# Kernel tuning notes

Hardware: AMD Instinct MI355X
Metric: run time of the kernel (lower is better)

Reference implementation:

```python
import jax, jax.numpy as jnp
import numpy as np

EPS = 1e-5
OUTPUT_BINS = 1000


def _act_quant(x):
    # per-token absmax int8 quantization (BitNet b1.58)
    scale = 127.0 / jnp.clip(jnp.max(jnp.abs(x), axis=-1, keepdims=True), EPS, None)
    return jnp.clip(jnp.round(x * scale), -128.0, 127.0) / scale


def _weight_quant(w):
    # ternary absmean quantization
    scale = 1.0 / jnp.clip(jnp.mean(jnp.abs(w)), EPS, None)
    return jnp.clip(jnp.round(w * scale), -1.0, 1.0) / scale


def _ste(x, q):
    return x + jax.lax.stop_gradient(q - x)


def bitlinear(x, w):
    xq = _ste(x, _act_quant(x))
    wq = _ste(w, _weight_quant(w))
    return jnp.einsum('bi,oi->bo', xq, wq)


def layernorm(x, g, b):
    mu = jnp.mean(x, axis=-1, keepdims=True)
    var = jnp.mean(jnp.square(x - mu), axis=-1, keepdims=True)
    return (x - mu) * jax.lax.rsqrt(var + EPS) * g + b


def setup_inputs() -> dict:
    key = jax.random.key(0)
    ks = jax.random.split(key, 5)
    B, D_IN, H = 4096, 1024, 4096
    return {
        'x': jax.random.normal(ks[0], (B, D_IN), dtype=jnp.float32),
        'W0': jax.random.normal(ks[1], (H, D_IN), dtype=jnp.float32) * 0.02,
        'W1': jax.random.normal(ks[2], (H, H), dtype=jnp.float32) * 0.02,
        'W2': jax.random.normal(ks[3], (H, H), dtype=jnp.float32) * 0.02,
        'W3': jax.random.normal(ks[4], (2 * OUTPUT_BINS, H), dtype=jnp.float32) * 0.02,
        'g0': jnp.ones((H,), jnp.float32), 'b0': jnp.zeros((H,), jnp.float32),
        'g1': jnp.ones((H,), jnp.float32), 'b1': jnp.zeros((H,), jnp.float32),
        'g2': jnp.ones((H,), jnp.float32), 'b2': jnp.zeros((H,), jnp.float32),
    }


def reference(x, W0, W1, W2, W3, g0, b0, g1, b1, g2, b2):
    h = jax.nn.silu(layernorm(bitlinear(x, W0), g0, b0))
    h = jax.nn.silu(layernorm(bitlinear(h, W1), g1, b1))
    h = jax.nn.silu(layernorm(bitlinear(h, W2), g2, b2))
    out = bitlinear(h, W3)                      # [B, 2*output_bins]
    mz_logits, int_logits = jnp.split(out, 2, axis=-1)
    mz_values = jax.nn.sigmoid(mz_logits) * (OUTPUT_BINS - 1) + 1.0
    intensities = jax.nn.sigmoid(int_logits) * 100.0
    return (mz_values, intensities)
```

## Files before the change

### kernel.cpp

```cpp
#include <hip/hip_runtime.h>
#include <cstdint>
#include <cstddef>

#define EPS 1e-5f

typedef __attribute__((ext_vector_type(4))) int int32x4;

__device__ __forceinline__ float blk_sum(float v, float* s4) {
    #pragma unroll
    for (int o = 32; o; o >>= 1) v += __shfl_down(v, o, 64);
    if ((threadIdx.x & 63) == 0) s4[threadIdx.x >> 6] = v;
    __syncthreads();
    v = s4[0] + s4[1] + s4[2] + s4[3];
    __syncthreads();
    return v;
}

__device__ __forceinline__ float blk_max(float v, float* s4) {
    #pragma unroll
    for (int o = 32; o; o >>= 1) v = fmaxf(v, __shfl_down(v, o, 64));
    if ((threadIdx.x & 63) == 0) s4[threadIdx.x >> 6] = v;
    __syncthreads();
    v = fmaxf(fmaxf(s4[0], s4[1]), fmaxf(s4[2], s4[3]));
    __syncthreads();
    return v;
}

__device__ __forceinline__ int pack4(float a, float b, float c, float d, float lo, float hi) {
    int x0 = (int)fminf(fmaxf(a, lo), hi);
    int x1 = (int)fminf(fmaxf(b, lo), hi);
    int x2 = (int)fminf(fmaxf(c, lo), hi);
    int x3 = (int)fminf(fmaxf(d, lo), hi);
    return (x0 & 255) | ((x1 & 255) << 8) | ((x2 & 255) << 16) | ((x3 & 255) << 24);
}

__global__ __launch_bounds__(256) void absmean_kernel(const float* __restrict__ w,
                                                      long long n4, float* __restrict__ out) {
    __shared__ float s4[4];
    const float4* w4 = (const float4*)w;
    float s = 0.f;
    for (long long i = (long long)blockIdx.x * 256 + threadIdx.x; i < n4;
         i += (long long)gridDim.x * 256) {
        float4 v = w4[i];
        s += fabsf(v.x) + fabsf(v.y) + fabsf(v.z) + fabsf(v.w);
    }
    s = blk_sum(s, s4);
    if (threadIdx.x == 0) atomicAdd(out, s);
}

__global__ __launch_bounds__(256) void wquant_kernel(const float* __restrict__ w,
                                                     int* __restrict__ q, long long n4,
                                                     const float* __restrict__ sump, float invN) {
    float mean = fmaxf(sump[0] * invN, EPS);
    float scale = 1.f / mean;
    const float4* w4 = (const float4*)w;
    for (long long i = (long long)blockIdx.x * 256 + threadIdx.x; i < n4;
         i += (long long)gridDim.x * 256) {
        float4 v = w4[i];
        q[i] = pack4(rintf(v.x * scale), rintf(v.y * scale),
                     rintf(v.z * scale), rintf(v.w * scale), -1.f, 1.f);
    }
}

__global__ __launch_bounds__(256) void actquant_kernel(const float* __restrict__ x,
                                                       int* __restrict__ q,
                                                       float* __restrict__ inv_s) {
    __shared__ float s4[4];
    int row = blockIdx.x;
    const float4* xr = (const float4*)(x + (size_t)row * 1024);
    float4 v = xr[threadIdx.x];
    float m = fmaxf(fmaxf(fabsf(v.x), fabsf(v.y)), fmaxf(fabsf(v.z), fabsf(v.w)));
    m = blk_max(m, s4);
    m = fmaxf(m, EPS);
    float scale = 127.f / m;
    if (threadIdx.x == 0) inv_s[row] = m / 127.f;
    q[(size_t)row * 256 + threadIdx.x] =
        pack4(rintf(v.x * scale), rintf(v.y * scale),
              rintf(v.z * scale), rintf(v.w * scale), -128.f, 127.f);
}

__global__ __launch_bounds__(256) void ln_silu_quant_kernel(const float* __restrict__ h,
                                                            const float* __restrict__ g,
                                                            const float* __restrict__ b,
                                                            int* __restrict__ q,
                                                            float* __restrict__ inv_s) {
    __shared__ float s4[4];
    int row = blockIdx.x;
    const float4* xr = (const float4*)(h + (size_t)row * 4096);
    float4 v[4];
    float sum = 0.f, sq = 0.f;
    #pragma unroll
    for (int i = 0; i < 4; i++) {
        v[i] = xr[threadIdx.x + i * 256];
        sum += v[i].x + v[i].y + v[i].z + v[i].w;
        sq += v[i].x * v[i].x + v[i].y * v[i].y + v[i].z * v[i].z + v[i].w * v[i].w;
    }
    sum = blk_sum(sum, s4);
    sq = blk_sum(sq, s4);
    float mu = sum * (1.f / 4096.f);
    float var = sq * (1.f / 4096.f) - mu * mu;
    float rs = rsqrtf(var + EPS);
    const float4* g4 = (const float4*)g;
    const float4* b4 = (const float4*)b;
    float amax = 0.f;
    #pragma unroll
    for (int i = 0; i < 4; i++) {
        float4 gg = g4[threadIdx.x + i * 256];
        float4 bb = b4[threadIdx.x + i * 256];
        float y0 = (v[i].x - mu) * rs * gg.x + bb.x;
        float y1 = (v[i].y - mu) * rs * gg.y + bb.y;
        float y2 = (v[i].z - mu) * rs * gg.z + bb.z;
        float y3 = (v[i].w - mu) * rs * gg.w + bb.w;
        v[i].x = y0 / (1.f + expf(-y0));
        v[i].y = y1 / (1.f + expf(-y1));
        v[i].z = y2 / (1.f + expf(-y2));
        v[i].w = y3 / (1.f + expf(-y3));
        amax = fmaxf(amax, fmaxf(fmaxf(fabsf(v[i].x), fabsf(v[i].y)),
                                 fmaxf(fabsf(v[i].z), fabsf(v[i].w))));
    }
    amax = blk_max(amax, s4);
    amax = fmaxf(amax, EPS);
    float scale = 127.f / amax;
    if (threadIdx.x == 0) inv_s[row] = amax / 127.f;
    #pragma unroll
    for (int i = 0; i < 4; i++) {
        q[(size_t)row * 1024 + threadIdx.x + i * 256] =
            pack4(rintf(v[i].x * scale), rintf(v[i].y * scale),
                  rintf(v[i].z * scale), rintf(v[i].w * scale), -128.f, 127.f);
    }
}

__device__ __forceinline__ void load_lds16(const void* g, void* l) {
    __builtin_amdgcn_global_load_lds((__attribute__((address_space(1))) void*)(g),
                                     (__attribute__((address_space(3))) void*)(l), 16, 0, 0);
}

template <int MODE>
__global__ __launch_bounds__(256, 2) void gemm_i8_kernel(
    const char* __restrict__ A, const char* __restrict__ B,
    const float* __restrict__ inv_s, const float* __restrict__ wsum, float invWN,
    int K, float* __restrict__ out) {
    __shared__ __align__(16) char lA[128 * 64];
    __shared__ __align__(16) char lB[128 * 64];
    const int t = threadIdx.x;
    const int lane = t & 63;
    const int wave = t >> 6;
    const int bm = blockIdx.y * 128, bn = blockIdx.x * 128;
    const int wr = (wave >> 1) * 64, wc = (wave & 1) * 64;

    int32x4 acc[4][4] = {};

    const int r0 = t >> 2;
    const int c0 = (t & 3) * 16;
    const char* gA0 = A + (size_t)(bm + r0) * K + c0;
    const char* gA1 = A + (size_t)(bm + r0 + 64) * K + c0;
    const char* gB0 = B + (size_t)(bn + r0) * K + c0;
    const char* gB1 = B + (size_t)(bn + r0 + 64) * K + c0;
    char* sA0 = lA + t * 16;
    char* sA1 = lA + 4096 + t * 16;
    char* sB0 = lB + t * 16;
    char* sB1 = lB + 4096 + t * 16;

    const int fr = lane & 15;
    const int fq = lane >> 4;

    for (int k0 = 0; k0 < K; k0 += 64) {
        load_lds16(gA0 + k0, sA0);
        load_lds16(gA1 + k0, sA1);
        load_lds16(gB0 + k0, sB0);
        load_lds16(gB1 + k0, sB1);
        __syncthreads();

        int32x4 af[4], bf[4];
        #pragma unroll
        for (int mt = 0; mt < 4; mt++)
            af[mt] = *(const int32x4*)(lA + (wr + mt * 16 + fr) * 64 + fq * 16);
        #pragma unroll
        for (int nt = 0; nt < 4; nt++)
            bf[nt] = *(const int32x4*)(lB + (wc + nt * 16 + fr) * 64 + fq * 16);
        #pragma unroll
        for (int mt = 0; mt < 4; mt++) {
            #pragma unroll
            for (int nt = 0; nt < 4; nt++) {
                acc[mt][nt] =
                    __builtin_amdgcn_mfma_i32_16x16x64_i8(af[mt], bf[nt], acc[mt][nt], 0, 0, 0);
            }
        }
        __syncthreads();
    }

    const float wmean = fmaxf(wsum[0] * invWN, EPS);
    #pragma unroll
    for (int mt = 0; mt < 4; mt++) {
        #pragma unroll
        for (int rg = 0; rg < 4; rg++) {
            int gr = bm + wr + mt * 16 + fq * 4 + rg;
            float rowscale = inv_s[gr] * wmean;
            #pragma unroll
            for (int nt = 0; nt < 4; nt++) {
                int gc = bn + wc + nt * 16 + fr;
                float v = (float)acc[mt][nt][rg] * rowscale;
                if (MODE == 0) {
                    out[(size_t)gr * 4096 + gc] = v;
                } else {
                    if (gc < 2000) {
                        float sg = 1.f / (1.f + expf(-v));
                        if (gc < 1000)
                            out[(size_t)gr * 1000 + gc] = sg * 999.f + 1.f;
                        else
                            out[(size_t)4096 * 1000 + (size_t)gr * 1000 + (gc - 1000)] =
                                sg * 100.f;
                    }
                }
            }
        }
    }
}

extern "C" void kernel_launch(void* const* d_in, const int* in_sizes, int n_in,
                              void* d_out, int out_size, void* d_ws, size_t ws_size,
                              hipStream_t stream) {
    const float* x  = (const float*)d_in[0];
    const float* W0 = (const float*)d_in[1];
    const float* W1 = (const float*)d_in[2];
    const float* W2 = (const float*)d_in[3];
    const float* W3 = (const float*)d_in[4];
    const float* g0 = (const float*)d_in[5];
    const float* b0 = (const float*)d_in[6];
    const float* g1 = (const float*)d_in[7];
    const float* b1 = (const float*)d_in[8];
    const float* g2 = (const float*)d_in[9];
    const float* b2 = (const float*)d_in[10];
    float* out = (float*)d_out;

    char* ws = (char*)d_ws;
    size_t off = 0;
    auto alloc = [&](size_t bytes) -> char* {
        char* p = ws + off;
        off = (off + bytes + 255) & ~(size_t)255;
        return p;
    };
    float* sums = (float*)alloc(4 * sizeof(float));
    float* inv0 = (float*)alloc(4096 * 4);
    float* inv1 = (float*)alloc(4096 * 4);
    float* inv2 = (float*)alloc(4096 * 4);
    float* inv3 = (float*)alloc(4096 * 4);
    char* wq0 = alloc(4096ll * 1024);
    char* wq1 = alloc(4096ll * 4096);
    char* wq2 = alloc(4096ll * 4096);
    char* wq3 = alloc(2048ll * 4096);
    char* a0  = alloc(4096ll * 1024);
    char* a1  = alloc(4096ll * 4096);
    char* a2  = alloc(4096ll * 4096);
    float* h  = (float*)alloc(4096ll * 4096 * 4);
    char* a3 = a1;

    const long long n0 = 4096ll * 1024, n1 = 4096ll * 4096, n2 = 4096ll * 4096,
                    n3 = 2000ll * 4096;

    hipMemsetAsync(sums, 0, 4 * sizeof(float), stream);
    hipMemsetAsync(wq3, 0, 2048ll * 4096, stream);

    absmean_kernel<<<1024, 256, 0, stream>>>(W0, n0 / 4, sums + 0);
    absmean_kernel<<<2048, 256, 0, stream>>>(W1, n1 / 4, sums + 1);
    absmean_kernel<<<2048, 256, 0, stream>>>(W2, n2 / 4, sums + 2);
    absmean_kernel<<<1024, 256, 0, stream>>>(W3, n3 / 4, sums + 3);

    wquant_kernel<<<1024, 256, 0, stream>>>(W0, (int*)wq0, n0 / 4, sums + 0, 1.f / (float)n0);
    wquant_kernel<<<2048, 256, 0, stream>>>(W1, (int*)wq1, n1 / 4, sums + 1, 1.f / (float)n1);
    wquant_kernel<<<2048, 256, 0, stream>>>(W2, (int*)wq2, n2 / 4, sums + 2, 1.f / (float)n2);
    wquant_kernel<<<1024, 256, 0, stream>>>(W3, (int*)wq3, n3 / 4, sums + 3, 1.f / (float)n3);

    actquant_kernel<<<4096, 256, 0, stream>>>(x, (int*)a0, inv0);

    gemm_i8_kernel<0><<<dim3(32, 32), 256, 0, stream>>>(a0, wq0, inv0, sums + 0,
                                                        1.f / (float)n0, 1024, h);
    ln_silu_quant_kernel<<<4096, 256, 0, stream>>>(h, g0, b0, (int*)a1, inv1);

    gemm_i8_kernel<0><<<dim3(32, 32), 256, 0, stream>>>(a1, wq1, inv1, sums + 1,
                                                        1.f / (float)n1, 4096, h);
    ln_silu_quant_kernel<<<4096, 256, 0, stream>>>(h, g1, b1, (int*)a2, inv2);

    gemm_i8_kernel<0><<<dim3(32, 32), 256, 0, stream>>>(a2, wq2, inv2, sums + 2,
                                                        1.f / (float)n2, 4096, h);
    ln_silu_quant_kernel<<<4096, 256, 0, stream>>>(h, g2, b2, (int*)a3, inv3);

    gemm_i8_kernel<1><<<dim3(16, 32), 256, 0, stream>>>(a3, wq3, inv3, sums + 3,
                                                        1.f / (float)n3, 4096, out);
}
```

Baseline: 636.4 us.

## Switch GEMMs to 32x32 MFMA, store hidden as bf16, merge weight-quant launches

Several changes land together. The int8 GEMM now uses 32x32x32 MFMA tiles with 2x2 accumulators and a launch-bounds hint of 4 blocks. Hidden activations are written as bf16 instead of fp32, which halves the intermediate traffic read by the layernorm kernel; that kernel also loads contiguously and fuses its two reductions. The four absmean launches and four weight-quant launches each become one merged launch, and the memset of the padded W3 buffer is folded into the quant kernel. The bf16 intermediate loses precision before layernorm and quantization, which may shift some rounded int8 values.

```diff
diff --git a/kernel.cpp b/kernel.cpp
--- a/kernel.cpp
+++ b/kernel.cpp
@@ -1,10 +1,12 @@
 #include <hip/hip_runtime.h>
+#include <hip/hip_bf16.h>
 #include <cstdint>
 #include <cstddef>
 
 #define EPS 1e-5f
 
 typedef __attribute__((ext_vector_type(4))) int int32x4;
+typedef __attribute__((ext_vector_type(16))) int int32x16;
 
 __device__ __forceinline__ float blk_sum(float v, float* s4) {
     #pragma unroll
@@ -14,6 +16,22 @@
     v = s4[0] + s4[1] + s4[2] + s4[3];
     __syncthreads();
     return v;
+}
+
+__device__ __forceinline__ void blk_sum2(float& a, float& b, float* s8) {
+    #pragma unroll
+    for (int o = 32; o; o >>= 1) {
+        a += __shfl_down(a, o, 64);
+        b += __shfl_down(b, o, 64);
+    }
+    if ((threadIdx.x & 63) == 0) {
+        s8[threadIdx.x >> 6] = a;
+        s8[4 + (threadIdx.x >> 6)] = b;
+    }
+    __syncthreads();
+    a = s8[0] + s8[1] + s8[2] + s8[3];
+    b = s8[4] + s8[5] + s8[6] + s8[7];
+    __syncthreads();
 }
 
 __device__ __forceinline__ float blk_max(float v, float* s4) {
@@ -34,31 +52,52 @@
     return (x0 & 255) | ((x1 & 255) << 8) | ((x2 & 255) << 16) | ((x3 & 255) << 24);
 }
 
-__global__ __launch_bounds__(256) void absmean_kernel(const float* __restrict__ w,
-                                                      long long n4, float* __restrict__ out) {
+__device__ __forceinline__ float bflo(unsigned u) { return __uint_as_float(u << 16); }
+__device__ __forceinline__ float bfhi(unsigned u) { return __uint_as_float(u & 0xffff0000u); }
+
+__global__ __launch_bounds__(256) void absmean_all_kernel(
+    const float* __restrict__ W0, const float* __restrict__ W1,
+    const float* __restrict__ W2, const float* __restrict__ W3,
+    float* __restrict__ sums) {
     __shared__ float s4[4];
+    const float* w; long long n4; int sidx, nb, lb;
+    int bx = blockIdx.x;
+    if (bx < 1024)      { w = W0; n4 = 1048576;  sidx = 0; nb = 1024; lb = bx; }
+    else if (bx < 3072) { w = W1; n4 = 4194304;  sidx = 1; nb = 2048; lb = bx - 1024; }
+    else if (bx < 5120) { w = W2; n4 = 4194304;  sidx = 2; nb = 2048; lb = bx - 3072; }
+    else                { w = W3; n4 = 2048000;  sidx = 3; nb = 1024; lb = bx - 5120; }
     const float4* w4 = (const float4*)w;
     float s = 0.f;
-    for (long long i = (long long)blockIdx.x * 256 + threadIdx.x; i < n4;
-         i += (long long)gridDim.x * 256) {
+    for (long long i = (long long)lb * 256 + threadIdx.x; i < n4; i += (long long)nb * 256) {
         float4 v = w4[i];
         s += fabsf(v.x) + fabsf(v.y) + fabsf(v.z) + fabsf(v.w);
     }
     s = blk_sum(s, s4);
-    if (threadIdx.x == 0) atomicAdd(out, s);
-}
-
-__global__ __launch_bounds__(256) void wquant_kernel(const float* __restrict__ w,
-                                                     int* __restrict__ q, long long n4,
-                                                     const float* __restrict__ sump, float invN) {
-    float mean = fmaxf(sump[0] * invN, EPS);
+    if (threadIdx.x == 0) atomicAdd(&sums[sidx], s);
+}
+
+__global__ __launch_bounds__(256) void wquant_all_kernel(
+    const float* __restrict__ W0, const float* __restrict__ W1,
+    const float* __restrict__ W2, const float* __restrict__ W3,
+    int* __restrict__ q0, int* __restrict__ q1, int* __restrict__ q2, int* __restrict__ q3,
+    const float* __restrict__ sums) {
+    const float* w; int* q; long long n4, pn4; int sidx, nb, lb; float invN;
+    int bx = blockIdx.x;
+    if (bx < 1024)      { w = W0; q = q0; n4 = 1048576;  pn4 = 1048576; sidx = 0; nb = 1024; lb = bx;        invN = 1.f / 4194304.f; }
+    else if (bx < 3072) { w = W1; q = q1; n4 = 4194304;  pn4 = 4194304; sidx = 1; nb = 2048; lb = bx - 1024; invN = 1.f / 16777216.f; }
+    else if (bx < 5120) { w = W2; q = q2; n4 = 4194304;  pn4 = 4194304; sidx = 2; nb = 2048; lb = bx - 3072; invN = 1.f / 16777216.f; }
+    else                { w = W3; q = q3; n4 = 2048000;  pn4 = 2097152; sidx = 3; nb = 1024; lb = bx - 5120; invN = 1.f / 8192000.f; }
+    float mean = fmaxf(sums[sidx] * invN, EPS);
     float scale = 1.f / mean;
     const float4* w4 = (const float4*)w;
-    for (long long i = (long long)blockIdx.x * 256 + threadIdx.x; i < n4;
-         i += (long long)gridDim.x * 256) {
-        float4 v = w4[i];
-        q[i] = pack4(rintf(v.x * scale), rintf(v.y * scale),
-                     rintf(v.z * scale), rintf(v.w * scale), -1.f, 1.f);
+    for (long long i = (long long)lb * 256 + threadIdx.x; i < pn4; i += (long long)nb * 256) {
+        if (i < n4) {
+            float4 v = w4[i];
+            q[i] = pack4(rintf(v.x * scale), rintf(v.y * scale),
+                         rintf(v.z * scale), rintf(v.w * scale), -1.f, 1.f);
+        } else {
+            q[i] = 0;
+        }
     }
 }
 
@@ -79,24 +118,25 @@
               rintf(v.z * scale), rintf(v.w * scale), -128.f, 127.f);
 }
 
-__global__ __launch_bounds__(256) void ln_silu_quant_kernel(const float* __restrict__ h,
+__global__ __launch_bounds__(256) void ln_silu_quant_kernel(const ushort* __restrict__ h,
                                                             const float* __restrict__ g,
                                                             const float* __restrict__ b,
                                                             int* __restrict__ q,
                                                             float* __restrict__ inv_s) {
-    __shared__ float s4[4];
+    __shared__ float s8[8];
     int row = blockIdx.x;
-    const float4* xr = (const float4*)(h + (size_t)row * 4096);
-    float4 v[4];
+    int t = threadIdx.x;
+    const uint4* hr = (const uint4*)(h + (size_t)row * 4096);
+    uint4 p0 = hr[t * 2], p1 = hr[t * 2 + 1];
+    float f[16];
+    f[0] = bflo(p0.x); f[1] = bfhi(p0.x); f[2] = bflo(p0.y); f[3] = bfhi(p0.y);
+    f[4] = bflo(p0.z); f[5] = bfhi(p0.z); f[6] = bflo(p0.w); f[7] = bfhi(p0.w);
+    f[8] = bflo(p1.x); f[9] = bfhi(p1.x); f[10] = bflo(p1.y); f[11] = bfhi(p1.y);
+    f[12] = bflo(p1.z); f[13] = bfhi(p1.z); f[14] = bflo(p1.w); f[15] = bfhi(p1.w);
     float sum = 0.f, sq = 0.f;
     #pragma unroll
-    for (int i = 0; i < 4; i++) {
-        v[i] = xr[threadIdx.x + i * 256];
-        sum += v[i].x + v[i].y + v[i].z + v[i].w;
-        sq += v[i].x * v[i].x + v[i].y * v[i].y + v[i].z * v[i].z + v[i].w * v[i].w;
-    }
-    sum = blk_sum(sum, s4);
-    sq = blk_sum(sq, s4);
+    for (int i = 0; i < 16; i++) { sum += f[i]; sq += f[i] * f[i]; }
+    blk_sum2(sum, sq, s8);
     float mu = sum * (1.f / 4096.f);
     float var = sq * (1.f / 4096.f) - mu * mu;
     float rs = rsqrtf(var + EPS);
@@ -105,29 +145,29 @@
     float amax = 0.f;
     #pragma unroll
     for (int i = 0; i < 4; i++) {
-        float4 gg = g4[threadIdx.x + i * 256];
-        float4 bb = b4[threadIdx.x + i * 256];
-        float y0 = (v[i].x - mu) * rs * gg.x + bb.x;
-        float y1 = (v[i].y - mu) * rs * gg.y + bb.y;
-        float y2 = (v[i].z - mu) * rs * gg.z + bb.z;
-        float y3 = (v[i].w - mu) * rs * gg.w + bb.w;
-        v[i].x = y0 / (1.f + expf(-y0));
-        v[i].y = y1 / (1.f + expf(-y1));
-        v[i].z = y2 / (1.f + expf(-y2));
-        v[i].w = y3 / (1.f + expf(-y3));
-        amax = fmaxf(amax, fmaxf(fmaxf(fabsf(v[i].x), fabsf(v[i].y)),
-                                 fmaxf(fabsf(v[i].z), fabsf(v[i].w))));
-    }
-    amax = blk_max(amax, s4);
+        float4 gg = g4[t * 4 + i];
+        float4 bb = b4[t * 4 + i];
+        float y0 = (f[i * 4 + 0] - mu) * rs * gg.x + bb.x;
+        float y1 = (f[i * 4 + 1] - mu) * rs * gg.y + bb.y;
+        float y2 = (f[i * 4 + 2] - mu) * rs * gg.z + bb.z;
+        float y3 = (f[i * 4 + 3] - mu) * rs * gg.w + bb.w;
+        f[i * 4 + 0] = y0 / (1.f + expf(-y0));
+        f[i * 4 + 1] = y1 / (1.f + expf(-y1));
+        f[i * 4 + 2] = y2 / (1.f + expf(-y2));
+        f[i * 4 + 3] = y3 / (1.f + expf(-y3));
+    }
+    #pragma unroll
+    for (int i = 0; i < 16; i++) amax = fmaxf(amax, fabsf(f[i]));
+    amax = blk_max(amax, s8);
     amax = fmaxf(amax, EPS);
     float scale = 127.f / amax;
-    if (threadIdx.x == 0) inv_s[row] = amax / 127.f;
-    #pragma unroll
-    for (int i = 0; i < 4; i++) {
-        q[(size_t)row * 1024 + threadIdx.x + i * 256] =
-            pack4(rintf(v[i].x * scale), rintf(v[i].y * scale),
-                  rintf(v[i].z * scale), rintf(v[i].w * scale), -128.f, 127.f);
-    }
+    if (t == 0) inv_s[row] = amax / 127.f;
+    int4 o;
+    o.x = pack4(rintf(f[0] * scale), rintf(f[1] * scale), rintf(f[2] * scale), rintf(f[3] * scale), -128.f, 127.f);
+    o.y = pack4(rintf(f[4] * scale), rintf(f[5] * scale), rintf(f[6] * scale), rintf(f[7] * scale), -128.f, 127.f);
+    o.z = pack4(rintf(f[8] * scale), rintf(f[9] * scale), rintf(f[10] * scale), rintf(f[11] * scale), -128.f, 127.f);
+    o.w = pack4(rintf(f[12] * scale), rintf(f[13] * scale), rintf(f[14] * scale), rintf(f[15] * scale), -128.f, 127.f);
+    ((int4*)((char*)q + (size_t)row * 4096))[t] = o;
 }
 
 __device__ __forceinline__ void load_lds16(const void* g, void* l) {
@@ -136,10 +176,10 @@
 }
 
 template <int MODE>
-__global__ __launch_bounds__(256, 2) void gemm_i8_kernel(
+__global__ __launch_bounds__(256, 4) void gemm_i8_kernel(
     const char* __restrict__ A, const char* __restrict__ B,
     const float* __restrict__ inv_s, const float* __restrict__ wsum, float invWN,
-    int K, float* __restrict__ out) {
+    int K, void* __restrict__ outp) {
     __shared__ __align__(16) char lA[128 * 64];
     __shared__ __align__(16) char lB[128 * 64];
     const int t = threadIdx.x;
@@ -148,7 +188,7 @@
     const int bm = blockIdx.y * 128, bn = blockIdx.x * 128;
     const int wr = (wave >> 1) * 64, wc = (wave & 1) * 64;
 
-    int32x4 acc[4][4] = {};
+    int32x16 acc[2][2] = {};
 
     const int r0 = t >> 2;
     const int c0 = (t & 3) * 16;
@@ -161,8 +201,12 @@
     char* sB0 = lB + t * 16;
     char* sB1 = lB + 4096 + t * 16;
 
-    const int fr = lane & 15;
-    const int fq = lane >> 4;
+    const int r = lane & 31;
+    const int q = lane >> 5;
+    const char* pA0 = lA + (wr + r) * 64 + q * 16;
+    const char* pA1 = pA0 + 32 * 64;
+    const char* pB0 = lB + (wc + r) * 64 + q * 16;
+    const char* pB1 = pB0 + 32 * 64;
 
     for (int k0 = 0; k0 < K; k0 += 64) {
         load_lds16(gA0 + k0, sA0);
@@ -171,40 +215,37 @@
         load_lds16(gB1 + k0, sB1);
         __syncthreads();
 
-        int32x4 af[4], bf[4];
         #pragma unroll
-        for (int mt = 0; mt < 4; mt++)
-            af[mt] = *(const int32x4*)(lA + (wr + mt * 16 + fr) * 64 + fq * 16);
-        #pragma unroll
-        for (int nt = 0; nt < 4; nt++)
-            bf[nt] = *(const int32x4*)(lB + (wc + nt * 16 + fr) * 64 + fq * 16);
-        #pragma unroll
-        for (int mt = 0; mt < 4; mt++) {
-            #pragma unroll
-            for (int nt = 0; nt < 4; nt++) {
-                acc[mt][nt] =
-                    __builtin_amdgcn_mfma_i32_16x16x64_i8(af[mt], bf[nt], acc[mt][nt], 0, 0, 0);
-            }
+        for (int ks = 0; ks < 2; ks++) {
+            int32x4 a0 = *(const int32x4*)(pA0 + ks * 32);
+            int32x4 a1 = *(const int32x4*)(pA1 + ks * 32);
+            int32x4 b0 = *(const int32x4*)(pB0 + ks * 32);
+            int32x4 b1 = *(const int32x4*)(pB1 + ks * 32);
+            acc[0][0] = __builtin_amdgcn_mfma_i32_32x32x32_i8(a0, b0, acc[0][0], 0, 0, 0);
+            acc[0][1] = __builtin_amdgcn_mfma_i32_32x32x32_i8(a0, b1, acc[0][1], 0, 0, 0);
+            acc[1][0] = __builtin_amdgcn_mfma_i32_32x32x32_i8(a1, b0, acc[1][0], 0, 0, 0);
+            acc[1][1] = __builtin_amdgcn_mfma_i32_32x32x32_i8(a1, b1, acc[1][1], 0, 0, 0);
         }
         __syncthreads();
     }
 
     const float wmean = fmaxf(wsum[0] * invWN, EPS);
     #pragma unroll
-    for (int mt = 0; mt < 4; mt++) {
+    for (int mt = 0; mt < 2; mt++) {
         #pragma unroll
-        for (int rg = 0; rg < 4; rg++) {
-            int gr = bm + wr + mt * 16 + fq * 4 + rg;
+        for (int reg = 0; reg < 16; reg++) {
+            int gr = bm + wr + mt * 32 + 4 * q + (reg & 3) + 8 * (reg >> 2);
             float rowscale = inv_s[gr] * wmean;
             #pragma unroll
-            for (int nt = 0; nt < 4; nt++) {
-                int gc = bn + wc + nt * 16 + fr;
-                float v = (float)acc[mt][nt][rg] * rowscale;
+            for (int nt = 0; nt < 2; nt++) {
+                int gc = bn + wc + nt * 32 + r;
+                float v = (float)acc[mt][nt][reg] * rowscale;
                 if (MODE == 0) {
-                    out[(size_t)gr * 4096 + gc] = v;
+                    ((__hip_bfloat16*)outp)[(size_t)gr * 4096 + gc] = __float2bfloat16(v);
                 } else {
                     if (gc < 2000) {
                         float sg = 1.f / (1.f + expf(-v));
+                        float* out = (float*)outp;
                         if (gc < 1000)
                             out[(size_t)gr * 1000 + gc] = sg * 999.f + 1.f;
                         else
@@ -252,39 +293,28 @@
     char* a0  = alloc(4096ll * 1024);
     char* a1  = alloc(4096ll * 4096);
     char* a2  = alloc(4096ll * 4096);
-    float* h  = (float*)alloc(4096ll * 4096 * 4);
+    char* h   = alloc(4096ll * 4096 * 2);
     char* a3 = a1;
 
-    const long long n0 = 4096ll * 1024, n1 = 4096ll * 4096, n2 = 4096ll * 4096,
-                    n3 = 2000ll * 4096;
-
     hipMemsetAsync(sums, 0, 4 * sizeof(float), stream);
-    hipMemsetAsync(wq3, 0, 2048ll * 4096, stream);
-
-    absmean_kernel<<<1024, 256, 0, stream>>>(W0, n0 / 4, sums + 0);
-    absmean_kernel<<<2048, 256, 0, stream>>>(W1, n1 / 4, sums + 1);
-    absmean_kernel<<<2048, 256, 0, stream>>>(W2, n2 / 4, sums + 2);
-    absmean_kernel<<<1024, 256, 0, stream>>>(W3, n3 / 4, sums + 3);
-
-    wquant_kernel<<<1024, 256, 0, stream>>>(W0, (int*)wq0, n0 / 4, sums + 0, 1.f / (float)n0);
-    wquant_kernel<<<2048, 256, 0, stream>>>(W1, (int*)wq1, n1 / 4, sums + 1, 1.f / (float)n1);
-    wquant_kernel<<<2048, 256, 0, stream>>>(W2, (int*)wq2, n2 / 4, sums + 2, 1.f / (float)n2);
-    wquant_kernel<<<1024, 256, 0, stream>>>(W3, (int*)wq3, n3 / 4, sums + 3, 1.f / (float)n3);
-
+
+    absmean_all_kernel<<<6144, 256, 0, stream>>>(W0, W1, W2, W3, sums);
     actquant_kernel<<<4096, 256, 0, stream>>>(x, (int*)a0, inv0);
+    wquant_all_kernel<<<6144, 256, 0, stream>>>(W0, W1, W2, W3, (int*)wq0, (int*)wq1,
+                                                (int*)wq2, (int*)wq3, sums);
 
     gemm_i8_kernel<0><<<dim3(32, 32), 256, 0, stream>>>(a0, wq0, inv0, sums + 0,
-                                                        1.f / (float)n0, 1024, h);
-    ln_silu_quant_kernel<<<4096, 256, 0, stream>>>(h, g0, b0, (int*)a1, inv1);
+                                                        1.f / 4194304.f, 1024, h);
+    ln_silu_quant_kernel<<<4096, 256, 0, stream>>>((const ushort*)h, g0, b0, (int*)a1, inv1);
 
     gemm_i8_kernel<0><<<dim3(32, 32), 256, 0, stream>>>(a1, wq1, inv1, sums + 1,
-                                                        1.f / (float)n1, 4096, h);
-    ln_silu_quant_kernel<<<4096, 256, 0, stream>>>(h, g1, b1, (int*)a2, inv2);
+                                                        1.f / 16777216.f, 4096, h);
+    ln_silu_quant_kernel<<<4096, 256, 0, stream>>>((const ushort*)h, g1, b1, (int*)a2, inv2);
 
     gemm_i8_kernel<0><<<dim3(32, 32), 256, 0, stream>>>(a2, wq2, inv2, sums + 2,
-                                                        1.f / (float)n2, 4096, h);
-    ln_silu_quant_kernel<<<4096, 256, 0, stream>>>(h, g2, b2, (int*)a3, inv3);
+                                                        1.f / 16777216.f, 4096, h);
+    ln_silu_quant_kernel<<<4096, 256, 0, stream>>>((const ushort*)h, g2, b2, (int*)a3, inv3);
 
     gemm_i8_kernel<1><<<dim3(16, 32), 256, 0, stream>>>(a3, wq3, inv3, sums + 3,
-                                                        1.f / (float)n3, 4096, out);
-}
+                                                        1.f / 8192000.f, 4096, out);
+}
```

Measured after the change: 612.4 us. 3.8% less time.
